# Kernel optimization log

Hardware: AMD Instinct MI355X
Metric: run time of the kernel (lower is better)

Reference implementation:

```python
import jax, jax.numpy as jnp
import numpy as np

NUM_ITERS = 3  # num_iterations init arg


def squash(t, axis):
    # scale = ||t||^2 / (1+||t||^2); out = scale * t / ||t||
    sn = jnp.sum(t * t, axis=axis, keepdims=True)
    return (sn / (1.0 + sn)) * t / jnp.sqrt(sn)


def setup_inputs() -> dict:
    key = jax.random.key(0)
    k1, k2, k3 = jax.random.split(key, 3)
    B, I, O, DI, DO = 2048, 64, 32, 16, 16
    x = jax.random.normal(k1, (B, DI, I), dtype=jnp.float32)
    route_weights = jax.random.normal(k2, (O, I, DO, DI), dtype=jnp.float32)
    noise = 0.01 * jax.random.normal(k3, (O, I, DO, DI), dtype=jnp.float32)
    return {"x": x, "route_weights": route_weights, "noise": noise}


def reference(x, route_weights, noise):
    # random=True branch: perturbed routing weights
    W = route_weights + noise                      # [O,I,do,di]
    xt = jnp.transpose(x, (0, 2, 1))               # [B,I,di]
    # priors[b,o,i,d] = sum_e W[o,i,d,e] * xt[b,i,e]  (trailing singleton dim dropped)
    priors = jnp.einsum('oide,bie->boid', W, xt)   # [B,O,I,do]
    logits = jnp.zeros_like(priors)
    out = None
    for it in range(NUM_ITERS):
        probs = jax.nn.softmax(logits, axis=2)     # over input capsules I
        out = squash(jnp.sum(probs * priors, axis=2, keepdims=True), axis=3)  # [B,O,1,do]
        if it != NUM_ITERS - 1:
            logits = logits + priors * out         # routing-by-agreement update
    out = out[:, :, 0, :]                          # squeeze -> [B,O,do]
    # unsqueeze(0).transpose(2,1) -> [1,O,B,do]
    return jnp.transpose(out[None], (0, 2, 1, 3))
```

## Files before the change

### kernel.cpp

```cpp
#include <hip/hip_runtime.h>


#define THREADS 512

__global__ __launch_bounds__(256) void wsum_kernel(
    const float* __restrict__ rw, const float* __restrict__ ns,
    float* __restrict__ w2)
{
    const int i = blockIdx.x * 256 + threadIdx.x;
    const float4 a = reinterpret_cast<const float4*>(rw)[i];
    const float4 n = reinterpret_cast<const float4*>(ns)[i];
    float4 r;
    r.x = a.x + n.x;  r.y = a.y + n.y;  r.z = a.z + n.z;  r.w = a.w + n.w;
    reinterpret_cast<float4*>(w2)[i] = r;
}

template <bool PRE>
__global__ __launch_bounds__(THREADS) void routing_kernel(
    const float* __restrict__ x,
    const float* __restrict__ rw,
    const float* __restrict__ ns,
    float* __restrict__ out)
{
    extern __shared__ float lds[];
    float* xlds = lds + 8192;

    const int tid  = threadIdx.x;
    const int w    = tid >> 6;
    const int lane = tid & 63;

    const int o  = blockIdx.x >> 5;
    const int bc = blockIdx.x & 31;
    const int bbase = bc * 64;

    float wq0[16], wq1[16];
    {
        const int base = (o * 64 + lane) * 256 + w * 32;
        #pragma unroll
        for (int eq = 0; eq < 4; ++eq) {
            if (PRE) {
                const float4 a0 = *reinterpret_cast<const float4*>(rw + base + eq * 4);
                wq0[4*eq+0] = a0.x;  wq0[4*eq+1] = a0.y;
                wq0[4*eq+2] = a0.z;  wq0[4*eq+3] = a0.w;
                const float4 a1 = *reinterpret_cast<const float4*>(rw + base + 16 + eq * 4);
                wq1[4*eq+0] = a1.x;  wq1[4*eq+1] = a1.y;
                wq1[4*eq+2] = a1.z;  wq1[4*eq+3] = a1.w;
            } else {
                const float4 a0 = *reinterpret_cast<const float4*>(rw + base + eq * 4);
                const float4 n0 = *reinterpret_cast<const float4*>(ns + base + eq * 4);
                wq0[4*eq+0] = a0.x + n0.x;  wq0[4*eq+1] = a0.y + n0.y;
                wq0[4*eq+2] = a0.z + n0.z;  wq0[4*eq+3] = a0.w + n0.w;
                const float4 a1 = *reinterpret_cast<const float4*>(rw + base + 16 + eq * 4);
                const float4 n1 = *reinterpret_cast<const float4*>(ns + base + 16 + eq * 4);
                wq1[4*eq+0] = a1.x + n1.x;  wq1[4*eq+1] = a1.y + n1.y;
                wq1[4*eq+2] = a1.z + n1.z;  wq1[4*eq+3] = a1.w + n1.w;
            }
        }
    }

    const int d0 = 2 * w, d1 = 2 * w + 1;
    float* pw0 = lds + d0 * 64 + ((((lane >> 2) ^ (d0 & 7)) << 2) | (lane & 3));
    float* pw1 = lds + d1 * 64 + ((((lane >> 2) ^ (d1 & 7)) << 2) | (lane & 3));

    const int qB  = lane >> 4;
    const int dB  = lane & 15;
    const int swz = dB & 7;
    const float4* prbase = reinterpret_cast<const float4*>(lds) + (w * 16 + dB) * 16;
    const float4* pr0 = prbase + ((4 * qB + 0) ^ swz);
    const float4* pr1 = prbase + ((4 * qB + 1) ^ swz);
    const float4* pr2 = prbase + ((4 * qB + 2) ^ swz);
    const float4* pr3 = prbase + ((4 * qB + 3) ^ swz);

    const float* xrb = xlds + lane * 16 + ((lane >> 3) << 2);

    const int il = lane & 15, ih = lane >> 4;
    float* xwb = xlds + w * 1056 + il * 64 + ((il >> 1) << 2) + ih;
    float* xw0 = xwb + 0;
    float* xw1 = xwb + 4;
    float* xw2 = xwb + 8;
    float* xw3 = xwb + 12;

    const float4* xsrc0 = reinterpret_cast<const float4*>(x) + bbase * 256
                        + (w * 256 + lane);

    const int outbase = (o * 2048 + bbase + w) * 16 + dB;

    float4 xb0 = xsrc0[0];
    float4 xb1 = xsrc0[64];
    float4 xb2 = xsrc0[128];
    float4 xb3 = xsrc0[192];
    xw0[0] = xb0.x;  xw0[16] = xb0.y;  xw0[32] = xb0.z;  xw0[48] = xb0.w;
    xw1[0] = xb1.x;  xw1[16] = xb1.y;  xw1[32] = xb1.z;  xw1[48] = xb1.w;
    xw2[0] = xb2.x;  xw2[16] = xb2.y;  xw2[32] = xb2.z;  xw2[48] = xb2.w;
    xw3[0] = xb3.x;  xw3[16] = xb3.y;  xw3[32] = xb3.z;  xw3[48] = xb3.w;
    __syncthreads();

    #pragma unroll
    for (int s = 0; s < 8; ++s) {
        #pragma unroll
        for (int bb = 0; bb < 8; ++bb) {
            const float4 v0 = *reinterpret_cast<const float4*>(xrb + bb * 1056 + 0);
            const float4 v1 = *reinterpret_cast<const float4*>(xrb + bb * 1056 + 4);
            const float4 v2 = *reinterpret_cast<const float4*>(xrb + bb * 1056 + 8);
            const float4 v3 = *reinterpret_cast<const float4*>(xrb + bb * 1056 + 12);
            float a0 = 0.f, a1 = 0.f;
            a0 = fmaf(wq0[0],  v0.x, a0);  a1 = fmaf(wq1[0],  v0.x, a1);
            a0 = fmaf(wq0[1],  v0.y, a0);  a1 = fmaf(wq1[1],  v0.y, a1);
            a0 = fmaf(wq0[2],  v0.z, a0);  a1 = fmaf(wq1[2],  v0.z, a1);
            a0 = fmaf(wq0[3],  v0.w, a0);  a1 = fmaf(wq1[3],  v0.w, a1);
            a0 = fmaf(wq0[4],  v1.x, a0);  a1 = fmaf(wq1[4],  v1.x, a1);
            a0 = fmaf(wq0[5],  v1.y, a0);  a1 = fmaf(wq1[5],  v1.y, a1);
            a0 = fmaf(wq0[6],  v1.z, a0);  a1 = fmaf(wq1[6],  v1.z, a1);
            a0 = fmaf(wq0[7],  v1.w, a0);  a1 = fmaf(wq1[7],  v1.w, a1);
            a0 = fmaf(wq0[8],  v2.x, a0);  a1 = fmaf(wq1[8],  v2.x, a1);
            a0 = fmaf(wq0[9],  v2.y, a0);  a1 = fmaf(wq1[9],  v2.y, a1);
            a0 = fmaf(wq0[10], v2.z, a0);  a1 = fmaf(wq1[10], v2.z, a1);
            a0 = fmaf(wq0[11], v2.w, a0);  a1 = fmaf(wq1[11], v2.w, a1);
            a0 = fmaf(wq0[12], v3.x, a0);  a1 = fmaf(wq1[12], v3.x, a1);
            a0 = fmaf(wq0[13], v3.y, a0);  a1 = fmaf(wq1[13], v3.y, a1);
            a0 = fmaf(wq0[14], v3.z, a0);  a1 = fmaf(wq1[14], v3.z, a1);
            a0 = fmaf(wq0[15], v3.w, a0);  a1 = fmaf(wq1[15], v3.w, a1);
            pw0[bb * 1024] = a0;
            pw1[bb * 1024] = a1;
        }
        __syncthreads();

        float p[16];
        {
            const float4 v0 = *pr0, v1 = *pr1, v2 = *pr2, v3 = *pr3;
            p[0]=v0.x; p[1]=v0.y; p[2]=v0.z; p[3]=v0.w;
            p[4]=v1.x; p[5]=v1.y; p[6]=v1.z; p[7]=v1.w;
            p[8]=v2.x; p[9]=v2.y; p[10]=v2.z; p[11]=v2.w;
            p[12]=v3.x; p[13]=v3.y; p[14]=v3.z; p[15]=v3.w;
        }

        if (s < 7) {
            const float4* xsrc = xsrc0 + (s + 1) * 2048;
            xb0 = xsrc[0];  xb1 = xsrc[64];  xb2 = xsrc[128];  xb3 = xsrc[192];
        }

        float t0 = (p[0]+p[1]) + (p[2]+p[3]);
        float t1 = (p[4]+p[5]) + (p[6]+p[7]);
        float t2 = (p[8]+p[9]) + (p[10]+p[11]);
        float t3 = (p[12]+p[13]) + (p[14]+p[15]);
        float part = (t0 + t1) + (t2 + t3);
        part += __shfl_xor(part, 16);
        part += __shfl_xor(part, 32);
        float sv = part * (1.0f / 64.0f);

        float sn = sv * sv;
        sn += __shfl_xor(sn, 1); sn += __shfl_xor(sn, 2);
        sn += __shfl_xor(sn, 4); sn += __shfl_xor(sn, 8);
        float factor = __builtin_amdgcn_sqrtf(sn)
                     * __builtin_amdgcn_rcpf(1.0f + sn);
        float Vsum = sv * factor;

        #pragma unroll
        for (int it = 0; it < 2; ++it) {
            const float c = Vsum * 1.44269504089f;
            float e0, e1, e2, e3;
            float dd0, dd1, dd2, dd3, nn0, nn1, nn2, nn3;
            e0 = __builtin_amdgcn_exp2f(p[0] * c);
            e1 = __builtin_amdgcn_exp2f(p[1] * c);
            e2 = __builtin_amdgcn_exp2f(p[2] * c);
            e3 = __builtin_amdgcn_exp2f(p[3] * c);
            dd0 = e0; dd1 = e1; dd2 = e2; dd3 = e3;
            nn0 = e0 * p[0]; nn1 = e1 * p[1]; nn2 = e2 * p[2]; nn3 = e3 * p[3];
            e0 = __builtin_amdgcn_exp2f(p[4] * c);
            e1 = __builtin_amdgcn_exp2f(p[5] * c);
            e2 = __builtin_amdgcn_exp2f(p[6] * c);
            e3 = __builtin_amdgcn_exp2f(p[7] * c);
            dd0 += e0; dd1 += e1; dd2 += e2; dd3 += e3;
            nn0 = fmaf(e0, p[4], nn0); nn1 = fmaf(e1, p[5], nn1);
            nn2 = fmaf(e2, p[6], nn2); nn3 = fmaf(e3, p[7], nn3);
            e0 = __builtin_amdgcn_exp2f(p[8] * c);
            e1 = __builtin_amdgcn_exp2f(p[9] * c);
            e2 = __builtin_amdgcn_exp2f(p[10] * c);
            e3 = __builtin_amdgcn_exp2f(p[11] * c);
            dd0 += e0; dd1 += e1; dd2 += e2; dd3 += e3;
            nn0 = fmaf(e0, p[8], nn0);  nn1 = fmaf(e1, p[9], nn1);
            nn2 = fmaf(e2, p[10], nn2); nn3 = fmaf(e3, p[11], nn3);
            e0 = __builtin_amdgcn_exp2f(p[12] * c);
            e1 = __builtin_amdgcn_exp2f(p[13] * c);
            e2 = __builtin_amdgcn_exp2f(p[14] * c);
            e3 = __builtin_amdgcn_exp2f(p[15] * c);
            dd0 += e0; dd1 += e1; dd2 += e2; dd3 += e3;
            nn0 = fmaf(e0, p[12], nn0); nn1 = fmaf(e1, p[13], nn1);
            nn2 = fmaf(e2, p[14], nn2); nn3 = fmaf(e3, p[15], nn3);

            float den = (dd0 + dd1) + (dd2 + dd3);
            float num = (nn0 + nn1) + (nn2 + nn3);
            den += __shfl_xor(den, 16); den += __shfl_xor(den, 32);
            num += __shfl_xor(num, 16); num += __shfl_xor(num, 32);
            sv = num * __builtin_amdgcn_rcpf(den);
            sn = sv * sv;
            sn += __shfl_xor(sn, 1); sn += __shfl_xor(sn, 2);
            sn += __shfl_xor(sn, 4); sn += __shfl_xor(sn, 8);
            factor = __builtin_amdgcn_sqrtf(sn)
                   * __builtin_amdgcn_rcpf(1.0f + sn);
            Vsum += sv * factor;
        }

        if (qB == 0)
            out[outbase + s * 128] = sv * factor;

        if (s < 7) {
            xw0[0] = xb0.x;  xw0[16] = xb0.y;  xw0[32] = xb0.z;  xw0[48] = xb0.w;
            xw1[0] = xb1.x;  xw1[16] = xb1.y;  xw1[32] = xb1.z;  xw1[48] = xb1.w;
            xw2[0] = xb2.x;  xw2[16] = xb2.y;  xw2[32] = xb2.z;  xw2[48] = xb2.w;
            xw3[0] = xb3.x;  xw3[16] = xb3.y;  xw3[32] = xb3.z;  xw3[48] = xb3.w;
        }
        __syncthreads();
    }
}

extern "C" void kernel_launch(void* const* d_in, const int* in_sizes, int n_in,
                              void* d_out, int out_size, void* d_ws, size_t ws_size,
                              hipStream_t stream) {
    const float* x  = (const float*)d_in[0];
    const float* rw = (const float*)d_in[1];
    const float* ns = (const float*)d_in[2];
    float* out = (float*)d_out;
    (void)in_sizes; (void)n_in; (void)out_size;

    const int grid = 32 * 32;
    const size_t w2_bytes = 32u * 64u * 16u * 16u * sizeof(float);

    if (ws_size >= w2_bytes) {
        float* w2 = (float*)d_ws;
        wsum_kernel<<<512, 256, 0, stream>>>(rw, ns, w2);
        routing_kernel<true><<<grid, THREADS, 66560, stream>>>(x, w2, ns, out);
    } else {
        routing_kernel<false><<<grid, THREADS, 66560, stream>>>(x, rw, ns, out);
    }
}
```

Before: 76.59 us.

## Compute capsule priors with split-bf16 MFMA instead of scalar FP32 FMAs

Replaces the per-thread FP32 FMA loop that builds the priors with MFMA 16x16x32 bf16 instructions. Weights and x are split into high and low bf16 halves, so two MFMAs per tile approximate FP32 precision. The x staging in LDS is rebuilt as a packed bf16 layout with XOR swizzles, and the priors scatter back into LDS uses new swizzled indices. It also reduces the shared memory request, in exchange for extra split/pack ALU work and some loss of precision (the low-times-low term is dropped).

```diff
diff --git a/kernel.cpp b/kernel.cpp
--- a/kernel.cpp
+++ b/kernel.cpp
@@ -2,6 +2,16 @@
 
 
 #define THREADS 512
+
+typedef __attribute__((ext_vector_type(8))) short bf16x8;
+typedef __attribute__((ext_vector_type(4))) float f32x4;
+
+__device__ __forceinline__ unsigned hi_bits(float v) {
+    return __float_as_uint(v) & 0xFFFF0000u;
+}
+__device__ __forceinline__ unsigned lo_u(float v) {
+    return __float_as_uint(v - __uint_as_float(hi_bits(v)));
+}
 
 __global__ __launch_bounds__(256) void wsum_kernel(
     const float* __restrict__ rw, const float* __restrict__ ns,
@@ -23,7 +33,6 @@
     float* __restrict__ out)
 {
     extern __shared__ float lds[];
-    float* xlds = lds + 8192;
 
     const int tid  = threadIdx.x;
     const int w    = tid >> 6;
@@ -33,95 +42,121 @@
     const int bc = blockIdx.x & 31;
     const int bbase = bc * 64;
 
-    float wq0[16], wq1[16];
+    bf16x8 whi[8], wlo[8];
     {
-        const int base = (o * 64 + lane) * 256 + w * 32;
-        #pragma unroll
-        for (int eq = 0; eq < 4; ++eq) {
-            if (PRE) {
-                const float4 a0 = *reinterpret_cast<const float4*>(rw + base + eq * 4);
-                wq0[4*eq+0] = a0.x;  wq0[4*eq+1] = a0.y;
-                wq0[4*eq+2] = a0.z;  wq0[4*eq+3] = a0.w;
-                const float4 a1 = *reinterpret_cast<const float4*>(rw + base + 16 + eq * 4);
-                wq1[4*eq+0] = a1.x;  wq1[4*eq+1] = a1.y;
-                wq1[4*eq+2] = a1.z;  wq1[4*eq+3] = a1.w;
-            } else {
-                const float4 a0 = *reinterpret_cast<const float4*>(rw + base + eq * 4);
-                const float4 n0 = *reinterpret_cast<const float4*>(ns + base + eq * 4);
-                wq0[4*eq+0] = a0.x + n0.x;  wq0[4*eq+1] = a0.y + n0.y;
-                wq0[4*eq+2] = a0.z + n0.z;  wq0[4*eq+3] = a0.w + n0.w;
-                const float4 a1 = *reinterpret_cast<const float4*>(rw + base + 16 + eq * 4);
-                const float4 n1 = *reinterpret_cast<const float4*>(ns + base + 16 + eq * 4);
-                wq1[4*eq+0] = a1.x + n1.x;  wq1[4*eq+1] = a1.y + n1.y;
-                wq1[4*eq+2] = a1.z + n1.z;  wq1[4*eq+3] = a1.w + n1.w;
+        const int dW  = lane & 15;
+        const int eoW = (lane >> 4) & 1;
+        const int wb  = ((o * 64 + 8 * w) * 16 + dW) * 16 + eoW * 8;
+        #pragma unroll
+        for (int t = 0; t < 8; ++t) {
+            float4 f0 = *reinterpret_cast<const float4*>(rw + wb + t * 256);
+            float4 f1 = *reinterpret_cast<const float4*>(rw + wb + t * 256 + 4);
+            if (!PRE) {
+                const float4 n0 = *reinterpret_cast<const float4*>(ns + wb + t * 256);
+                const float4 n1 = *reinterpret_cast<const float4*>(ns + wb + t * 256 + 4);
+                f0.x += n0.x; f0.y += n0.y; f0.z += n0.z; f0.w += n0.w;
+                f1.x += n1.x; f1.y += n1.y; f1.z += n1.z; f1.w += n1.w;
             }
-        }
-    }
-
-    const int d0 = 2 * w, d1 = 2 * w + 1;
-    float* pw0 = lds + d0 * 64 + ((((lane >> 2) ^ (d0 & 7)) << 2) | (lane & 3));
-    float* pw1 = lds + d1 * 64 + ((((lane >> 2) ^ (d1 & 7)) << 2) | (lane & 3));
-
-    const int qB  = lane >> 4;
-    const int dB  = lane & 15;
-    const int swz = dB & 7;
+            whi[t][0] = (short)(__float_as_uint(f0.x) >> 16);
+            whi[t][1] = (short)(__float_as_uint(f0.y) >> 16);
+            whi[t][2] = (short)(__float_as_uint(f0.z) >> 16);
+            whi[t][3] = (short)(__float_as_uint(f0.w) >> 16);
+            whi[t][4] = (short)(__float_as_uint(f1.x) >> 16);
+            whi[t][5] = (short)(__float_as_uint(f1.y) >> 16);
+            whi[t][6] = (short)(__float_as_uint(f1.z) >> 16);
+            whi[t][7] = (short)(__float_as_uint(f1.w) >> 16);
+            wlo[t][0] = (short)(lo_u(f0.x) >> 16);
+            wlo[t][1] = (short)(lo_u(f0.y) >> 16);
+            wlo[t][2] = (short)(lo_u(f0.z) >> 16);
+            wlo[t][3] = (short)(lo_u(f0.w) >> 16);
+            wlo[t][4] = (short)(lo_u(f1.x) >> 16);
+            wlo[t][5] = (short)(lo_u(f1.y) >> 16);
+            wlo[t][6] = (short)(lo_u(f1.z) >> 16);
+            wlo[t][7] = (short)(lo_u(f1.w) >> 16);
+        }
+    }
+
+    const int ridx = ((lane & 7) << 2) | (((lane >> 4) & 1) << 1) | (lane >> 5);
+    const char* xt_rd = reinterpret_cast<const char*>(lds) + 32768
+                      + w * 4096 + ((ridx ^ (w & 7)) << 4);
+    const int kskew = (lane >> 3) & 7;
+    char* xt_wr = reinterpret_cast<char*>(lds) + 32768 + lane * 512;
+    const int ow00 = ((w * 4 + 0) ^ kskew) << 4;
+    const int ow01 = ((w * 4 + 1) ^ kskew) << 4;
+    const int ow10 = ((w * 4 + 2) ^ kskew) << 4;
+    const int ow11 = ((w * 4 + 3) ^ kskew) << 4;
+
+    const int bA  = lane & 15;
+    const int dqA = lane >> 4;
+    const bool act = (lane & 8) == 0;
+    const int g0 = (4 * (dqA & 1) + 0) ^ (bA & 7) ^ ((2 * dqA) & 7);
+    const int g1 = (4 * (dqA & 1) + 1) ^ (bA & 7) ^ ((2 * dqA) & 7);
+    const int g2 = (4 * (dqA & 1) + 2) ^ (bA & 7) ^ ((2 * dqA) & 7);
+    const int g3 = (4 * (dqA & 1) + 3) ^ (bA & 7) ^ ((2 * dqA) & 7);
+    float* prow0 = lds + (bA * 16 + 4 * dqA + 0) * 64;
+    float* prow1 = lds + (bA * 16 + 4 * dqA + 1) * 64;
+    float* prow2 = lds + (bA * 16 + 4 * dqA + 2) * 64;
+    float* prow3 = lds + (bA * 16 + 4 * dqA + 3) * 64;
+    const int w00 = 4 * ((2 * w + 0) ^ g0), w01 = 4 * ((2 * w + 1) ^ g0);
+    const int w10 = 4 * ((2 * w + 0) ^ g1), w11 = 4 * ((2 * w + 1) ^ g1);
+    const int w20 = 4 * ((2 * w + 0) ^ g2), w21 = 4 * ((2 * w + 1) ^ g2);
+    const int w30 = 4 * ((2 * w + 0) ^ g3), w31 = 4 * ((2 * w + 1) ^ g3);
+
+    const int qB = lane >> 4;
+    const int dB = lane & 15;
+    const int gR = (dB & 7) ^ (w & 7) ^ ((2 * (dB >> 2)) & 7);
     const float4* prbase = reinterpret_cast<const float4*>(lds) + (w * 16 + dB) * 16;
-    const float4* pr0 = prbase + ((4 * qB + 0) ^ swz);
-    const float4* pr1 = prbase + ((4 * qB + 1) ^ swz);
-    const float4* pr2 = prbase + ((4 * qB + 2) ^ swz);
-    const float4* pr3 = prbase + ((4 * qB + 3) ^ swz);
-
-    const float* xrb = xlds + lane * 16 + ((lane >> 3) << 2);
-
-    const int il = lane & 15, ih = lane >> 4;
-    float* xwb = xlds + w * 1056 + il * 64 + ((il >> 1) << 2) + ih;
-    float* xw0 = xwb + 0;
-    float* xw1 = xwb + 4;
-    float* xw2 = xwb + 8;
-    float* xw3 = xwb + 12;
-
-    const float4* xsrc0 = reinterpret_cast<const float4*>(x) + bbase * 256
-                        + (w * 256 + lane);
+    const float4* pr0 = prbase + ((4 * qB + 0) ^ gR);
+    const float4* pr1 = prbase + ((4 * qB + 1) ^ gR);
+    const float4* pr2 = prbase + ((4 * qB + 2) ^ gR);
+    const float4* pr3 = prbase + ((4 * qB + 3) ^ gR);
 
     const int outbase = (o * 2048 + bbase + w) * 16 + dB;
 
-    float4 xb0 = xsrc0[0];
-    float4 xb1 = xsrc0[64];
-    float4 xb2 = xsrc0[128];
-    float4 xb3 = xsrc0[192];
-    xw0[0] = xb0.x;  xw0[16] = xb0.y;  xw0[32] = xb0.z;  xw0[48] = xb0.w;
-    xw1[0] = xb1.x;  xw1[16] = xb1.y;  xw1[32] = xb1.z;  xw1[48] = xb1.w;
-    xw2[0] = xb2.x;  xw2[16] = xb2.y;  xw2[32] = xb2.z;  xw2[48] = xb2.w;
-    xw3[0] = xb3.x;  xw3[16] = xb3.y;  xw3[32] = xb3.z;  xw3[48] = xb3.w;
+    const float* xsrc = x + (bbase + w) * 1024 + lane;
+
+    {
+        float v[16];
+        #pragma unroll
+        for (int e = 0; e < 16; ++e) v[e] = xsrc[e * 64];
+        unsigned h0 = (__float_as_uint(v[0]) >> 16) | hi_bits(v[1]);
+        unsigned h1 = (__float_as_uint(v[2]) >> 16) | hi_bits(v[3]);
+        unsigned h2 = (__float_as_uint(v[4]) >> 16) | hi_bits(v[5]);
+        unsigned h3 = (__float_as_uint(v[6]) >> 16) | hi_bits(v[7]);
+        unsigned h4 = (__float_as_uint(v[8]) >> 16) | hi_bits(v[9]);
+        unsigned h5 = (__float_as_uint(v[10]) >> 16) | hi_bits(v[11]);
+        unsigned h6 = (__float_as_uint(v[12]) >> 16) | hi_bits(v[13]);
+        unsigned h7 = (__float_as_uint(v[14]) >> 16) | hi_bits(v[15]);
+        unsigned l0 = (lo_u(v[0]) >> 16) | (lo_u(v[1]) & 0xFFFF0000u);
+        unsigned l1 = (lo_u(v[2]) >> 16) | (lo_u(v[3]) & 0xFFFF0000u);
+        unsigned l2 = (lo_u(v[4]) >> 16) | (lo_u(v[5]) & 0xFFFF0000u);
+        unsigned l3 = (lo_u(v[6]) >> 16) | (lo_u(v[7]) & 0xFFFF0000u);
+        unsigned l4 = (lo_u(v[8]) >> 16) | (lo_u(v[9]) & 0xFFFF0000u);
+        unsigned l5 = (lo_u(v[10]) >> 16) | (lo_u(v[11]) & 0xFFFF0000u);
+        unsigned l6 = (lo_u(v[12]) >> 16) | (lo_u(v[13]) & 0xFFFF0000u);
+        unsigned l7 = (lo_u(v[14]) >> 16) | (lo_u(v[15]) & 0xFFFF0000u);
+        *reinterpret_cast<uint4*>(xt_wr + ow00) = make_uint4(h0, h1, h2, h3);
+        *reinterpret_cast<uint4*>(xt_wr + ow01) = make_uint4(l0, l1, l2, l3);
+        *reinterpret_cast<uint4*>(xt_wr + ow10) = make_uint4(h4, h5, h6, h7);
+        *reinterpret_cast<uint4*>(xt_wr + ow11) = make_uint4(l4, l5, l6, l7);
+    }
     __syncthreads();
 
     #pragma unroll
     for (int s = 0; s < 8; ++s) {
         #pragma unroll
-        for (int bb = 0; bb < 8; ++bb) {
-            const float4 v0 = *reinterpret_cast<const float4*>(xrb + bb * 1056 + 0);
-            const float4 v1 = *reinterpret_cast<const float4*>(xrb + bb * 1056 + 4);
-            const float4 v2 = *reinterpret_cast<const float4*>(xrb + bb * 1056 + 8);
-            const float4 v3 = *reinterpret_cast<const float4*>(xrb + bb * 1056 + 12);
-            float a0 = 0.f, a1 = 0.f;
-            a0 = fmaf(wq0[0],  v0.x, a0);  a1 = fmaf(wq1[0],  v0.x, a1);
-            a0 = fmaf(wq0[1],  v0.y, a0);  a1 = fmaf(wq1[1],  v0.y, a1);
-            a0 = fmaf(wq0[2],  v0.z, a0);  a1 = fmaf(wq1[2],  v0.z, a1);
-            a0 = fmaf(wq0[3],  v0.w, a0);  a1 = fmaf(wq1[3],  v0.w, a1);
-            a0 = fmaf(wq0[4],  v1.x, a0);  a1 = fmaf(wq1[4],  v1.x, a1);
-            a0 = fmaf(wq0[5],  v1.y, a0);  a1 = fmaf(wq1[5],  v1.y, a1);
-            a0 = fmaf(wq0[6],  v1.z, a0);  a1 = fmaf(wq1[6],  v1.z, a1);
-            a0 = fmaf(wq0[7],  v1.w, a0);  a1 = fmaf(wq1[7],  v1.w, a1);
-            a0 = fmaf(wq0[8],  v2.x, a0);  a1 = fmaf(wq1[8],  v2.x, a1);
-            a0 = fmaf(wq0[9],  v2.y, a0);  a1 = fmaf(wq1[9],  v2.y, a1);
-            a0 = fmaf(wq0[10], v2.z, a0);  a1 = fmaf(wq1[10], v2.z, a1);
-            a0 = fmaf(wq0[11], v2.w, a0);  a1 = fmaf(wq1[11], v2.w, a1);
-            a0 = fmaf(wq0[12], v3.x, a0);  a1 = fmaf(wq1[12], v3.x, a1);
-            a0 = fmaf(wq0[13], v3.y, a0);  a1 = fmaf(wq1[13], v3.y, a1);
-            a0 = fmaf(wq0[14], v3.z, a0);  a1 = fmaf(wq1[14], v3.z, a1);
-            a0 = fmaf(wq0[15], v3.w, a0);  a1 = fmaf(wq1[15], v3.w, a1);
-            pw0[bb * 1024] = a0;
-            pw1[bb * 1024] = a1;
+        for (int t = 0; t < 8; ++t) {
+            const bf16x8 bf = *reinterpret_cast<const bf16x8*>(xt_rd + t * 512);
+            f32x4 acc = {0.f, 0.f, 0.f, 0.f};
+            acc = __builtin_amdgcn_mfma_f32_16x16x32_bf16(wlo[t], bf, acc, 0, 0, 0);
+            acc = __builtin_amdgcn_mfma_f32_16x16x32_bf16(whi[t], bf, acc, 0, 0, 0);
+            if (act) {
+                const int m = t & 3;
+                prow0[((t >> 2) ? w01 : w00) + m] = acc[0];
+                prow1[((t >> 2) ? w11 : w10) + m] = acc[1];
+                prow2[((t >> 2) ? w21 : w20) + m] = acc[2];
+                prow3[((t >> 2) ? w31 : w30) + m] = acc[3];
+            }
         }
         __syncthreads();
 
@@ -134,9 +169,11 @@
             p[12]=v3.x; p[13]=v3.y; p[14]=v3.z; p[15]=v3.w;
         }
 
+        float se[8];
         if (s < 7) {
-            const float4* xsrc = xsrc0 + (s + 1) * 2048;
-            xb0 = xsrc[0];  xb1 = xsrc[64];  xb2 = xsrc[128];  xb3 = xsrc[192];
+            const float* xs = xsrc + (s + 1) * 8192;
+            se[0] = xs[0];   se[1] = xs[64];  se[2] = xs[128]; se[3] = xs[192];
+            se[4] = xs[256]; se[5] = xs[320]; se[6] = xs[384]; se[7] = xs[448];
         }
 
         float t0 = (p[0]+p[1]) + (p[2]+p[3]);
@@ -205,10 +242,30 @@
             out[outbase + s * 128] = sv * factor;
 
         if (s < 7) {
-            xw0[0] = xb0.x;  xw0[16] = xb0.y;  xw0[32] = xb0.z;  xw0[48] = xb0.w;
-            xw1[0] = xb1.x;  xw1[16] = xb1.y;  xw1[32] = xb1.z;  xw1[48] = xb1.w;
-            xw2[0] = xb2.x;  xw2[16] = xb2.y;  xw2[32] = xb2.z;  xw2[48] = xb2.w;
-            xw3[0] = xb3.x;  xw3[16] = xb3.y;  xw3[32] = xb3.z;  xw3[48] = xb3.w;
+            const float* xs = xsrc + (s + 1) * 8192;
+            float sl[8];
+            sl[0] = xs[512]; sl[1] = xs[576]; sl[2] = xs[640]; sl[3] = xs[704];
+            sl[4] = xs[768]; sl[5] = xs[832]; sl[6] = xs[896]; sl[7] = xs[960];
+            unsigned h0 = (__float_as_uint(se[0]) >> 16) | hi_bits(se[1]);
+            unsigned h1 = (__float_as_uint(se[2]) >> 16) | hi_bits(se[3]);
+            unsigned h2 = (__float_as_uint(se[4]) >> 16) | hi_bits(se[5]);
+            unsigned h3 = (__float_as_uint(se[6]) >> 16) | hi_bits(se[7]);
+            unsigned l0 = (lo_u(se[0]) >> 16) | (lo_u(se[1]) & 0xFFFF0000u);
+            unsigned l1 = (lo_u(se[2]) >> 16) | (lo_u(se[3]) & 0xFFFF0000u);
+            unsigned l2 = (lo_u(se[4]) >> 16) | (lo_u(se[5]) & 0xFFFF0000u);
+            unsigned l3 = (lo_u(se[6]) >> 16) | (lo_u(se[7]) & 0xFFFF0000u);
+            unsigned h4 = (__float_as_uint(sl[0]) >> 16) | hi_bits(sl[1]);
+            unsigned h5 = (__float_as_uint(sl[2]) >> 16) | hi_bits(sl[3]);
+            unsigned h6 = (__float_as_uint(sl[4]) >> 16) | hi_bits(sl[5]);
+            unsigned h7 = (__float_as_uint(sl[6]) >> 16) | hi_bits(sl[7]);
+            unsigned l4 = (lo_u(sl[0]) >> 16) | (lo_u(sl[1]) & 0xFFFF0000u);
+            unsigned l5 = (lo_u(sl[2]) >> 16) | (lo_u(sl[3]) & 0xFFFF0000u);
+            unsigned l6 = (lo_u(sl[4]) >> 16) | (lo_u(sl[5]) & 0xFFFF0000u);
+            unsigned l7 = (lo_u(sl[6]) >> 16) | (lo_u(sl[7]) & 0xFFFF0000u);
+            *reinterpret_cast<uint4*>(xt_wr + ow00) = make_uint4(h0, h1, h2, h3);
+            *reinterpret_cast<uint4*>(xt_wr + ow01) = make_uint4(l0, l1, l2, l3);
+            *reinterpret_cast<uint4*>(xt_wr + ow10) = make_uint4(h4, h5, h6, h7);
+            *reinterpret_cast<uint4*>(xt_wr + ow11) = make_uint4(l4, l5, l6, l7);
         }
         __syncthreads();
     }
@@ -229,8 +286,8 @@
     if (ws_size >= w2_bytes) {
         float* w2 = (float*)d_ws;
         wsum_kernel<<<512, 256, 0, stream>>>(rw, ns, w2);
-        routing_kernel<true><<<grid, THREADS, 66560, stream>>>(x, w2, ns, out);
+        routing_kernel<true><<<grid, THREADS, 65536, stream>>>(x, w2, ns, out);
     } else {
-        routing_kernel<false><<<grid, THREADS, 66560, stream>>>(x, rw, ns, out);
-    }
-}
+        routing_kernel<false><<<grid, THREADS, 65536, stream>>>(x, rw, ns, out);
+    }
+}
```

Result: slower. 96.41 us (+25.9%).
